# Kernel optimization log

Hardware: AMD Instinct MI355X
Metric: run time of the kernel (lower is better)

Reference implementation:

```python
import jax, jax.numpy as jnp
import numpy as np

B, N = 32768, 20            # batch nodes, temporal neighbors
NF, EF, TF = 172, 172, 100  # node / edge / time feature dims
E = NF + TF                 # query_dim = 272
KD = NF + EF + TF           # key_dim = 444
H = 2                       # heads
HD = E // H                 # head dim 136
OUT = NF                    # output_dimension defaults to n_node_features
NEG = jnp.float32(-1e30)


def setup_inputs() -> dict:
    key = jax.random.key(0)
    ks = jax.random.split(key, 20)
    s = 0.02
    return {
        "src_node_features": jax.random.normal(ks[0], (B, NF), jnp.float32),
        "src_time_features": jax.random.normal(ks[1], (B, 1, TF), jnp.float32),
        "neighbor_features": jax.random.normal(ks[2], (B, N, NF), jnp.float32),
        "neighbor_time_features": jax.random.normal(ks[3], (B, N, TF), jnp.float32),
        "edge_features": jax.random.normal(ks[4], (B, N, EF), jnp.float32),
        "neighbor_mask": jax.random.bernoulli(ks[5], 0.3, (B, N)),
        # nn.MultiheadAttention params (separate q/k/v projections since kdim!=embed_dim)
        "q_w": jax.random.normal(ks[6], (E, E), jnp.float32) * s,
        "k_w": jax.random.normal(ks[7], (E, KD), jnp.float32) * s,
        "v_w": jax.random.normal(ks[8], (E, KD), jnp.float32) * s,
        "q_b": jnp.zeros((E,), jnp.float32),
        "k_b": jnp.zeros((E,), jnp.float32),
        "v_b": jnp.zeros((E,), jnp.float32),
        "out_w": jax.random.normal(ks[9], (E, E), jnp.float32) * s,
        "out_b": jnp.zeros((E,), jnp.float32),
        # merger MLP: Linear(E+NF -> OUT), ReLU, Linear(OUT -> OUT)
        "m1_w": jax.random.normal(ks[10], (OUT, E + NF), jnp.float32) * s,
        "m1_b": jnp.zeros((OUT,), jnp.float32),
        "m2_w": jax.random.normal(ks[11], (OUT, OUT), jnp.float32) * s,
        "m2_b": jnp.zeros((OUT,), jnp.float32),
    }


def reference(src_node_features, src_time_features, neighbor_features,
              neighbor_time_features, edge_features, neighbor_mask,
              q_w, k_w, v_w, q_b, k_b, v_b, out_w, out_b,
              m1_w, m1_b, m2_w, m2_b):
    b = src_node_features.shape[0]
    # single query per node: [B, E]
    query = jnp.concatenate([src_node_features, src_time_features[:, 0, :]], axis=1)
    # keys/values: [B, N, KD]
    kv = jnp.concatenate([neighbor_features, edge_features, neighbor_time_features], axis=2)

    # nodes with no valid neighbor: unmask position 0 (matches torch clone/set trick)
    invalid = jnp.all(neighbor_mask, axis=1)                      # [B]
    mask = neighbor_mask.at[:, 0].set(
        jnp.where(invalid, False, neighbor_mask[:, 0]))

    q = (query @ q_w.T + q_b).reshape(b, H, HD)                   # [B,H,HD]
    k = (kv @ k_w.T + k_b).reshape(b, N, H, HD)                   # [B,N,H,HD]
    v = (kv @ v_w.T + v_b).reshape(b, N, H, HD)

    scores = jnp.einsum('bhd,bnhd->bhn', q, k) / jnp.sqrt(jnp.float32(HD))
    scores = jnp.where(mask[:, None, :], NEG, scores)
    attn = jax.nn.softmax(scores, axis=-1)                        # [B,H,N]
    attn_weights = attn.mean(axis=1)                              # averaged over heads [B,N]

    ctx = jnp.einsum('bhn,bnhd->bhd', attn, v).reshape(b, E)
    attn_out = ctx @ out_w.T + out_b                              # [B,E]
    attn_out = jnp.where(invalid[:, None], 0.0, attn_out)

    merged = jnp.concatenate([attn_out, src_node_features], axis=1)
    hidden = jax.nn.relu(merged @ m1_w.T + m1_b)
    output = hidden @ m2_w.T + m2_b                               # [B,OUT]
    return output, attn_weights
```

## Files before the change

### kernel.cpp

```cpp
#include <hip/hip_runtime.h>
#include <hip/hip_bf16.h>
#include <math.h>

#define NF 172
#define TF_ 100
#define EF 172
#define EDIM 272
#define KD 444
#define NNB 20
#define HD 136
#define OUT_D 172

typedef __attribute__((ext_vector_type(4))) float f32x4;
typedef __attribute__((ext_vector_type(8))) __bf16 bf16x8;
typedef __attribute__((ext_vector_type(4))) __bf16 bf16x4;

__global__ void sniff_k(const unsigned char* __restrict__ m, int* __restrict__ flag) {
    __shared__ int c1, c2;
    if (threadIdx.x == 0) { c1 = 0; c2 = 0; }
    __syncthreads();
    for (int k = 0; k < 4; ++k) {
        int p = threadIdx.x * 4 + k;
        unsigned char v = m[p];
        if ((p & 3) != 0 && v)          atomicOr(&c1, 1);
        if ((p & 3) == 3 && v == 0x3f)  atomicOr(&c2, 1);
    }
    __syncthreads();
    if (threadIdx.x == 0) flag[0] = c2 ? 2 : (c1 ? 1 : 0);
}

__global__ __launch_bounds__(256) void prep_k(
    const float* __restrict__ q_w, const float* __restrict__ k_w,
    const float* __restrict__ v_w, const float* __restrict__ q_b,
    const float* __restrict__ v_b, const float* __restrict__ out_w,
    const float* __restrict__ out_b,
    float* __restrict__ GT, float* __restrict__ gb,
    float* __restrict__ MT, float* __restrict__ mb)
{
    const int blk = blockIdx.x;
    const int tid = threadIdx.x;
    if (blk < 888) {
        const int j = blk, h = j / 444, jj = j - h * 444;
        for (int k = tid; k < 272; k += 256) {
            float acc = 0.f;
#pragma unroll 4
            for (int c = 0; c < 136; ++c)
                acc += q_w[(size_t)(h * 136 + c) * 272 + k] *
                       k_w[(size_t)(h * 136 + c) * 444 + jj];
            GT[(size_t)j * 272 + k] = acc;
        }
    } else if (blk < 888 + 272) {
        const int j = blk - 888;
        for (int r = tid; r < 888; r += 256) {
            const int h = r / 444, d = r - h * 444;
            float acc = 0.f;
#pragma unroll 4
            for (int c = 0; c < 136; ++c)
                acc += v_w[(size_t)(h * 136 + c) * 444 + d] *
                       out_w[(size_t)j * 272 + h * 136 + c];
            MT[(size_t)j * 888 + r] = acc;
        }
    } else if (blk < 888 + 272 + 4) {
        const int j = (blk - 888 - 272) * 256 + tid;
        if (j < 888) {
            const int h = j / 444, jj = j - h * 444;
            float acc = 0.f;
#pragma unroll 4
            for (int c = 0; c < 136; ++c)
                acc += q_b[h * 136 + c] * k_w[(size_t)(h * 136 + c) * 444 + jj];
            gb[j] = acc;
        }
    } else {
        const int j = (blk - 888 - 272 - 4) * 256 + tid;
        if (j < 272) {
            float acc = out_b[j];
#pragma unroll 4
            for (int e = 0; e < 272; ++e)
                acc += v_b[e] * out_w[(size_t)j * 272 + e];
            mb[j] = acc;
        }
    }
}

#define BKP 40

__global__ __launch_bounds__(256) void gemm_mfma_k(
    const float* __restrict__ A0, int a0_cols, int a0_stride,
    const float* __restrict__ A1, int a1_stride,
    const float* __restrict__ W, int w_stride,
    const float* __restrict__ bias,
    const float* __restrict__ invalf,
    int relu,
    float* __restrict__ C, int c_stride,
    int N, int K)
{
    __shared__ __bf16 As[2][128][BKP];
    __shared__ __bf16 Bs[2][128][BKP];

    const int tid  = threadIdx.x;
    const int lane = tid & 63;
    const int wv   = tid >> 6;
    const int wr   = wv >> 1;
    const int wc   = wv & 1;
    const int lr   = lane & 15;
    const int lg   = lane >> 4;
    const int m0   = blockIdx.x * 128;
    const int n0   = blockIdx.y * 128;

    f32x4 acc[4][4];
#pragma unroll
    for (int i = 0; i < 4; ++i)
#pragma unroll
        for (int j = 0; j < 4; ++j) acc[i][j] = (f32x4)(0.f);

    const int srow = tid >> 1;
    const int sch0 = (tid & 1) * 4;
    const float4 z4 = make_float4(0.f, 0.f, 0.f, 0.f);
    float4 va[4], vb[4];

#define LOAD_T(k0base) do {                                                   \
    _Pragma("unroll")                                                         \
    for (int i_ = 0; i_ < 4; ++i_) {                                          \
        const int k_ = (k0base) + (sch0 + i_) * 4;                            \
        va[i_] = z4; vb[i_] = z4;                                             \
        if (k_ < K) {                                                         \
            const float* p_ = (k_ < a0_cols)                                  \
                ? (A0 + (size_t)(m0 + srow) * a0_stride + k_)                 \
                : (A1 + (size_t)(m0 + srow) * a1_stride + (k_ - a0_cols));    \
            va[i_] = *(const float4*)p_;                                      \
            if ((n0 + srow) < N)                                              \
                vb[i_] = *(const float4*)(W + (size_t)(n0 + srow) * w_stride + k_); \
        }                                                                     \
    } } while (0)

#define STORE_T(bufi) do {                                                    \
    _Pragma("unroll")                                                         \
    for (int i_ = 0; i_ < 4; ++i_) {                                          \
        bf16x4 ta_, tb_;                                                      \
        ta_[0] = (__bf16)va[i_].x; ta_[1] = (__bf16)va[i_].y;                 \
        ta_[2] = (__bf16)va[i_].z; ta_[3] = (__bf16)va[i_].w;                 \
        tb_[0] = (__bf16)vb[i_].x; tb_[1] = (__bf16)vb[i_].y;                 \
        tb_[2] = (__bf16)vb[i_].z; tb_[3] = (__bf16)vb[i_].w;                 \
        *(bf16x4*)&As[bufi][srow][(sch0 + i_) * 4] = ta_;                     \
        *(bf16x4*)&Bs[bufi][srow][(sch0 + i_) * 4] = tb_;                     \
    } } while (0)

    const int ktiles = (K + 31) / 32;
    LOAD_T(0);
    STORE_T(0);
    __syncthreads();

    int cur = 0;
    for (int t = 0; t < ktiles; ++t) {
        const int more = (t + 1 < ktiles);
        if (more) LOAD_T((t + 1) * 32);

        bf16x8 af[4], bfr[4];
#pragma unroll
        for (int f = 0; f < 4; ++f) {
            af[f]  = *(const bf16x8*)&As[cur][wr * 64 + f * 16 + lr][lg * 8];
            bfr[f] = *(const bf16x8*)&Bs[cur][wc * 64 + f * 16 + lr][lg * 8];
        }
#pragma unroll
        for (int fm = 0; fm < 4; ++fm)
#pragma unroll
            for (int fn = 0; fn < 4; ++fn)
                acc[fm][fn] = __builtin_amdgcn_mfma_f32_16x16x32_bf16(
                    af[fm], bfr[fn], acc[fm][fn], 0, 0, 0);

        if (more) STORE_T(cur ^ 1);
        __syncthreads();
        cur ^= 1;
    }
#undef LOAD_T
#undef STORE_T

    float bv[4];
#pragma unroll
    for (int fn = 0; fn < 4; ++fn) {
        const int col = n0 + wc * 64 + fn * 16 + lr;
        bv[fn] = (bias && col < N) ? bias[col] : 0.f;
    }
#pragma unroll
    for (int fm = 0; fm < 4; ++fm) {
#pragma unroll
        for (int j = 0; j < 4; ++j) {
            const int row = m0 + wr * 64 + fm * 16 + lg * 4 + j;
            float zf = 1.f;
            if (invalf && invalf[row] != 0.f) zf = 0.f;
#pragma unroll
            for (int fn = 0; fn < 4; ++fn) {
                const int col = n0 + wc * 64 + fn * 16 + lr;
                if (col < N) {
                    float v = acc[fm][fn][j] + bv[fn];
                    if (relu) v = fmaxf(v, 0.f);
                    C[(size_t)row * c_stride + col] = v * zf;
                }
            }
        }
    }
}

__device__ __forceinline__ float dot4(float4 a, float4 b) {
    return a.x * b.x + a.y * b.y + a.z * b.z + a.w * b.w;
}

__global__ __launch_bounds__(256) void attn_flash2_k(
    const float* __restrict__ nf, const float* __restrict__ ef,
    const float* __restrict__ ntf,
    const unsigned char* __restrict__ maskp,
    const int* __restrict__ mode_p,
    const float* __restrict__ qk,
    float* __restrict__ wkv,
    float* __restrict__ invalf,
    float* __restrict__ attnw)
{
    __shared__ float  sc_lds[2][2][NNB];
    __shared__ float4 acc_lds[2][4][64];

    const int tid  = threadIdx.x;
    const int lane = tid & 63;
    const int wv   = tid >> 6;
    const int rw   = wv >> 1;
    const int hf   = wv & 1;
    const int b    = blockIdx.x * 2 + rw;
    const int mode = mode_p[0];

    int mv = 0;
    if (lane < NNB) {
        if (mode == 0)      mv = ((const int*)maskp)[(size_t)b * NNB + lane] != 0;
        else if (mode == 1) mv = maskp[(size_t)b * NNB + lane] != 0;
        else                mv = ((const float*)maskp)[(size_t)b * NNB + lane] != 0.f;
    }
    unsigned long long bal = __ballot(lane < NNB && mv);
    const int inv = ((bal & 0xFFFFFULL) == 0xFFFFFULL);
    if (inv && lane == 0) mv = 0;
    if (hf == 0 && lane == 0) invalf[b] = (float)inv;

    const float* qrow = qk + (size_t)b * 888;
    const float4 z4 = make_float4(0.f, 0.f, 0.f, 0.f);
    float4 q0a = *(const float4*)(qrow + lane * 4);
    float4 q1a = *(const float4*)(qrow + KD + lane * 4);
    float4 q0b = z4, q1b = z4;
    if (lane < 47) {
        q0b = *(const float4*)(qrow + (64 + lane) * 4);
        q1b = *(const float4*)(qrow + KD + (64 + lane) * 4);
    }

    const size_t rbase = (size_t)b * NNB + hf * 10;
    const float* pA;
    if (lane < 43) pA = nf + rbase * NF + lane * 4;
    else           pA = ef + rbase * EF + (lane - 43) * 4;
    const float* pB;
    int strideB;
    if (lane < 22) { pB = ef  + rbase * EF  + (21 + lane) * 4; strideB = EF;  }
    else           { pB = ntf + rbase * TF_ + (lane - 22) * 4; strideB = TF_; }

    float4 kA[10], kB[10];
#pragma unroll
    for (int s = 0; s < 10; ++s) {
        kA[s] = *(const float4*)pA; pA += NF;
        kB[s] = z4;
        if (lane < 47) { kB[s] = *(const float4*)pB; }
        pB += strideB;
    }

    float s0v[10], s1v[10];
#pragma unroll
    for (int s = 0; s < 10; ++s) {
        s0v[s] = dot4(q0a, kA[s]) + dot4(q0b, kB[s]);
        s1v[s] = dot4(q1a, kA[s]) + dot4(q1b, kB[s]);
    }
#pragma unroll
    for (int off = 32; off; off >>= 1) {
#pragma unroll
        for (int s = 0; s < 10; ++s) {
            s0v[s] += __shfl_xor(s0v[s], off);
            s1v[s] += __shfl_xor(s1v[s], off);
        }
    }

    const float scal = 0.08574929257125441f;
#pragma unroll
    for (int s = 0; s < 10; ++s) {
        const int g = hf * 10 + s;
        const int mn = __shfl(mv, g);
        s0v[s] = mn ? -1e30f : s0v[s] * scal;
        s1v[s] = mn ? -1e30f : s1v[s] * scal;
        if (lane == s) { sc_lds[rw][0][g] = s0v[s]; sc_lds[rw][1][g] = s1v[s]; }
    }
    __syncthreads();

    float m0 = -3.4e38f, m1 = -3.4e38f;
#pragma unroll
    for (int g = 0; g < NNB; ++g) {
        m0 = fmaxf(m0, sc_lds[rw][0][g]);
        m1 = fmaxf(m1, sc_lds[rw][1][g]);
    }
    float sum0 = 0.f, sum1 = 0.f;
#pragma unroll
    for (int g = 0; g < NNB; ++g) {
        sum0 += expf(sc_lds[rw][0][g] - m0);
        sum1 += expf(sc_lds[rw][1][g] - m1);
    }
    const float r0 = 1.f / sum0;
    const float r1 = 1.f / sum1;

    float4 a0a = z4, a0b = z4, a1a = z4, a1b = z4;
#pragma unroll
    for (int s = 0; s < 10; ++s) {
        const float w0 = expf(s0v[s] - m0) * r0;
        const float w1 = expf(s1v[s] - m1) * r1;
        a0a.x += w0 * kA[s].x; a0a.y += w0 * kA[s].y; a0a.z += w0 * kA[s].z; a0a.w += w0 * kA[s].w;
        a0b.x += w0 * kB[s].x; a0b.y += w0 * kB[s].y; a0b.z += w0 * kB[s].z; a0b.w += w0 * kB[s].w;
        a1a.x += w1 * kA[s].x; a1a.y += w1 * kA[s].y; a1a.z += w1 * kA[s].z; a1a.w += w1 * kA[s].w;
        a1b.x += w1 * kB[s].x; a1b.y += w1 * kB[s].y; a1b.z += w1 * kB[s].z; a1b.w += w1 * kB[s].w;
    }

    if (hf == 1) {
        acc_lds[rw][0][lane] = a0a;
        acc_lds[rw][1][lane] = a0b;
        acc_lds[rw][2][lane] = a1a;
        acc_lds[rw][3][lane] = a1b;
    }
    __syncthreads();
    if (hf == 0) {
        float4 p0a = acc_lds[rw][0][lane], p0b = acc_lds[rw][1][lane];
        float4 p1a = acc_lds[rw][2][lane], p1b = acc_lds[rw][3][lane];
        a0a.x += p0a.x; a0a.y += p0a.y; a0a.z += p0a.z; a0a.w += p0a.w;
        a0b.x += p0b.x; a0b.y += p0b.y; a0b.z += p0b.z; a0b.w += p0b.w;
        a1a.x += p1a.x; a1a.y += p1a.y; a1a.z += p1a.z; a1a.w += p1a.w;
        a1b.x += p1b.x; a1b.y += p1b.y; a1b.z += p1b.z; a1b.w += p1b.w;

        float* wrow = wkv + (size_t)b * 888;
        *(float4*)(wrow + lane * 4)      = a0a;
        *(float4*)(wrow + KD + lane * 4) = a1a;
        if (lane < 47) {
            *(float4*)(wrow + (64 + lane) * 4)      = a0b;
            *(float4*)(wrow + KD + (64 + lane) * 4) = a1b;
        }
#pragma unroll
        for (int g = 0; g < NNB; ++g) {
            if (lane == g)
                attnw[(size_t)b * NNB + g] =
                    0.5f * (expf(sc_lds[rw][0][g] - m0) * r0 +
                            expf(sc_lds[rw][1][g] - m1) * r1);
        }
    }
}

extern "C" void kernel_launch(void* const* d_in, const int* in_sizes, int n_in,
                              void* d_out, int out_size, void* d_ws, size_t ws_size,
                              hipStream_t stream) {
    const float* src_node = (const float*)d_in[0];
    const float* src_time = (const float*)d_in[1];
    const float* nfp      = (const float*)d_in[2];
    const float* ntfp     = (const float*)d_in[3];
    const float* efp      = (const float*)d_in[4];
    const unsigned char* maskp = (const unsigned char*)d_in[5];
    const float* q_w   = (const float*)d_in[6];
    const float* k_w   = (const float*)d_in[7];
    const float* v_w   = (const float*)d_in[8];
    const float* q_b   = (const float*)d_in[9];
    const float* v_b   = (const float*)d_in[11];
    const float* out_w = (const float*)d_in[12];
    const float* out_b = (const float*)d_in[13];
    const float* m1_w  = (const float*)d_in[14];
    const float* m1_b  = (const float*)d_in[15];
    const float* m2_w  = (const float*)d_in[16];
    const float* m2_b  = (const float*)d_in[17];

    const int B = in_sizes[0] / NF;

    float* ws   = (float*)d_ws;
    int*   flag = (int*)d_ws;
    float* qkb  = ws + 16;
    float* invb = qkb + (size_t)B * 888;
    float* aob  = invb + B;
    float* GT   = aob + (size_t)B * 272;
    float* gb   = GT + 888 * 272;
    float* MT   = gb + 888;
    float* mb   = MT + 272 * 888;
    float* hidb = qkb;
    float* outp  = (float*)d_out;
    float* attnw = outp + (size_t)B * OUT_D;

    const int gm = B / 128;

    sniff_k<<<1, 256, 0, stream>>>(maskp, flag);
    prep_k<<<1166, 256, 0, stream>>>(q_w, k_w, v_w, q_b, v_b, out_w, out_b,
                                     GT, gb, MT, mb);

    gemm_mfma_k<<<dim3(gm, 7), 256, 0, stream>>>(
        src_node, NF, NF, src_time, TF_,
        GT, 272, gb, nullptr, 0, qkb, 888, 888, 272);

    attn_flash2_k<<<B / 2, 256, 0, stream>>>(nfp, efp, ntfp, maskp, flag,
                                             qkb, qkb, invb, attnw);

    gemm_mfma_k<<<dim3(gm, 3), 256, 0, stream>>>(
        qkb, 888, 888, nullptr, 0,
        MT, 888, mb, invb, 0, aob, 272, 272, 888);

    gemm_mfma_k<<<dim3(gm, 2), 256, 0, stream>>>(
        aob, EDIM, EDIM, src_node, NF,
        m1_w, KD, m1_b, nullptr, 1, hidb, OUT_D, OUT_D, KD);

    gemm_mfma_k<<<dim3(gm, 2), 256, 0, stream>>>(
        hidb, OUT_D, OUT_D, nullptr, 0,
        m2_w, OUT_D, m2_b, nullptr, 0, outp, OUT_D, OUT_D, OUT_D);
}
```

Baseline: 718.3 us.

## Fold out-projection into merger weights, split attention across four waves per node

Precomputes a combined weight W2 = m1_w[:, :272] · out_w · v_w per head, which folds the attention output projection into the first merger GEMM and removes one full B×888×272 GEMM plus its intermediate buffer. Invalid rows are handled with a separate bias vector (m1_b) instead of zeroing. The attention kernel now runs one node per block with four waves each covering five neighbors. It uses DPP-based wave reductions, exp2 with a pre-scaled log2e constant, and deferred normalization. The GEMM also gets a swizzled block index for L2 locality. The trade-off is more weight-preprocessing work and a small change in rounding order in the bf16 GEMM.

```diff
diff --git a/kernel.cpp b/kernel.cpp
--- a/kernel.cpp
+++ b/kernel.cpp
@@ -15,6 +15,8 @@
 typedef __attribute__((ext_vector_type(8))) __bf16 bf16x8;
 typedef __attribute__((ext_vector_type(4))) __bf16 bf16x4;
 
+#define SC2 0.12371009f
+
 __global__ void sniff_k(const unsigned char* __restrict__ m, int* __restrict__ flag) {
     __shared__ int c1, c2;
     if (threadIdx.x == 0) { c1 = 0; c2 = 0; }
@@ -29,13 +31,13 @@
     if (threadIdx.x == 0) flag[0] = c2 ? 2 : (c1 ? 1 : 0);
 }
 
-__global__ __launch_bounds__(256) void prep_k(
+__global__ __launch_bounds__(256) void prep1_k(
     const float* __restrict__ q_w, const float* __restrict__ k_w,
-    const float* __restrict__ v_w, const float* __restrict__ q_b,
-    const float* __restrict__ v_b, const float* __restrict__ out_w,
-    const float* __restrict__ out_b,
+    const float* __restrict__ q_b, const float* __restrict__ v_b,
+    const float* __restrict__ out_w, const float* __restrict__ out_b,
+    const float* __restrict__ m1_w,
     float* __restrict__ GT, float* __restrict__ gb,
-    float* __restrict__ MT, float* __restrict__ mb)
+    float* __restrict__ OW2, float* __restrict__ mb)
 {
     const int blk = blockIdx.x;
     const int tid = threadIdx.x;
@@ -49,19 +51,17 @@
                        k_w[(size_t)(h * 136 + c) * 444 + jj];
             GT[(size_t)j * 272 + k] = acc;
         }
-    } else if (blk < 888 + 272) {
+    } else if (blk < 1060) {
         const int j = blk - 888;
-        for (int r = tid; r < 888; r += 256) {
-            const int h = r / 444, d = r - h * 444;
+        for (int k = tid; k < 272; k += 256) {
             float acc = 0.f;
 #pragma unroll 4
-            for (int c = 0; c < 136; ++c)
-                acc += v_w[(size_t)(h * 136 + c) * 444 + d] *
-                       out_w[(size_t)j * 272 + h * 136 + c];
-            MT[(size_t)j * 888 + r] = acc;
-        }
-    } else if (blk < 888 + 272 + 4) {
-        const int j = (blk - 888 - 272) * 256 + tid;
+            for (int e = 0; e < 272; ++e)
+                acc += m1_w[(size_t)j * 444 + e] * out_w[(size_t)e * 272 + k];
+            OW2[(size_t)j * 272 + k] = acc;
+        }
+    } else if (blk < 1064) {
+        const int j = (blk - 1060) * 256 + tid;
         if (j < 888) {
             const int h = j / 444, jj = j - h * 444;
             float acc = 0.f;
@@ -71,13 +71,45 @@
             gb[j] = acc;
         }
     } else {
-        const int j = (blk - 888 - 272 - 4) * 256 + tid;
-        if (j < 272) {
+        for (int j = tid; j < 272; j += 256) {
             float acc = out_b[j];
 #pragma unroll 4
             for (int e = 0; e < 272; ++e)
                 acc += v_b[e] * out_w[(size_t)j * 272 + e];
             mb[j] = acc;
+        }
+    }
+}
+
+__global__ __launch_bounds__(256) void prep2_k(
+    const float* __restrict__ v_w, const float* __restrict__ m1_w,
+    const float* __restrict__ m1_b,
+    const float* __restrict__ OW2, const float* __restrict__ mb,
+    float* __restrict__ W2, float* __restrict__ bias_v)
+{
+    const int blk = blockIdx.x;
+    const int tid = threadIdx.x;
+    if (blk < 172) {
+        const int j = blk;
+        for (int r = tid; r < 888; r += 256) {
+            const int h = (r >= 444);
+            const int d = r - h * 444;
+            float acc = 0.f;
+#pragma unroll 4
+            for (int c = 0; c < 136; ++c)
+                acc += v_w[(size_t)(h * 136 + c) * 444 + d] *
+                       OW2[(size_t)j * 272 + h * 136 + c];
+            W2[(size_t)j * 1060 + r] = acc;
+        }
+        for (int k = tid; k < 172; k += 256)
+            W2[(size_t)j * 1060 + 888 + k] = m1_w[(size_t)j * 444 + 272 + k];
+    } else {
+        for (int j = tid; j < 172; j += 256) {
+            float acc = m1_b[j];
+#pragma unroll 4
+            for (int e = 0; e < 272; ++e)
+                acc += m1_w[(size_t)j * 444 + e] * mb[e];
+            bias_v[j] = acc;
         }
     }
 }
@@ -89,6 +121,7 @@
     const float* __restrict__ A1, int a1_stride,
     const float* __restrict__ W, int w_stride,
     const float* __restrict__ bias,
+    const float* __restrict__ bias_inv,
     const float* __restrict__ invalf,
     int relu,
     float* __restrict__ C, int c_stride,
@@ -104,8 +137,15 @@
     const int wc   = wv & 1;
     const int lr   = lane & 15;
     const int lg   = lane >> 4;
-    const int m0   = blockIdx.x * 128;
-    const int n0   = blockIdx.y * 128;
+
+    const int nt   = gridDim.y;
+    const int nwg  = gridDim.x * nt;
+    const int lid  = blockIdx.x + blockIdx.y * gridDim.x;
+    const int swz  = (lid & 7) * (nwg >> 3) + (lid >> 3);
+    const int xt   = swz / nt;
+    const int yt   = swz - xt * nt;
+    const int m0   = xt * 128;
+    const int n0   = yt * 128;
 
     f32x4 acc[4][4];
 #pragma unroll
@@ -175,26 +215,26 @@
 #undef LOAD_T
 #undef STORE_T
 
-    float bv[4];
+    float bv[4], bvi[4];
 #pragma unroll
     for (int fn = 0; fn < 4; ++fn) {
         const int col = n0 + wc * 64 + fn * 16 + lr;
-        bv[fn] = (bias && col < N) ? bias[col] : 0.f;
+        bv[fn]  = (bias && col < N) ? bias[col] : 0.f;
+        bvi[fn] = (bias_inv && col < N) ? bias_inv[col] : bv[fn];
     }
 #pragma unroll
     for (int fm = 0; fm < 4; ++fm) {
 #pragma unroll
         for (int j = 0; j < 4; ++j) {
             const int row = m0 + wr * 64 + fm * 16 + lg * 4 + j;
-            float zf = 1.f;
-            if (invalf && invalf[row] != 0.f) zf = 0.f;
+            const bool bad = invalf && invalf[row] != 0.f;
 #pragma unroll
             for (int fn = 0; fn < 4; ++fn) {
                 const int col = n0 + wc * 64 + fn * 16 + lr;
                 if (col < N) {
-                    float v = acc[fm][fn][j] + bv[fn];
+                    float v = acc[fm][fn][j] + (bad ? bvi[fn] : bv[fn]);
                     if (relu) v = fmaxf(v, 0.f);
-                    C[(size_t)row * c_stride + col] = v * zf;
+                    C[(size_t)row * c_stride + col] = v;
                 }
             }
         }
@@ -205,7 +245,22 @@
     return a.x * b.x + a.y * b.y + a.z * b.z + a.w * b.w;
 }
 
-__global__ __launch_bounds__(256) void attn_flash2_k(
+__device__ __forceinline__ float wave_allsum(float x) {
+    int t;
+    t = __builtin_amdgcn_update_dpp(0, __float_as_int(x), 0x128, 0xf, 0xf, true);
+    x += __int_as_float(t);
+    t = __builtin_amdgcn_update_dpp(0, __float_as_int(x), 0x124, 0xf, 0xf, true);
+    x += __int_as_float(t);
+    t = __builtin_amdgcn_update_dpp(0, __float_as_int(x), 0x122, 0xf, 0xf, true);
+    x += __int_as_float(t);
+    t = __builtin_amdgcn_update_dpp(0, __float_as_int(x), 0x121, 0xf, 0xf, true);
+    x += __int_as_float(t);
+    x += __shfl_xor(x, 16);
+    x += __shfl_xor(x, 32);
+    return x;
+}
+
+__global__ __launch_bounds__(256) void attn_flash3_k(
     const float* __restrict__ nf, const float* __restrict__ ef,
     const float* __restrict__ ntf,
     const unsigned char* __restrict__ maskp,
@@ -215,15 +270,14 @@
     float* __restrict__ invalf,
     float* __restrict__ attnw)
 {
-    __shared__ float  sc_lds[2][2][NNB];
-    __shared__ float4 acc_lds[2][4][64];
+    __shared__ float  sc[2][NNB];
+    __shared__ float  lmax[4][2], lsum[4][2];
+    __shared__ float4 accx[3][4][64];
 
     const int tid  = threadIdx.x;
     const int lane = tid & 63;
-    const int wv   = tid >> 6;
-    const int rw   = wv >> 1;
-    const int hf   = wv & 1;
-    const int b    = blockIdx.x * 2 + rw;
+    const int w    = tid >> 6;
+    const int b    = blockIdx.x;
     const int mode = mode_p[0];
 
     int mv = 0;
@@ -232,10 +286,10 @@
         else if (mode == 1) mv = maskp[(size_t)b * NNB + lane] != 0;
         else                mv = ((const float*)maskp)[(size_t)b * NNB + lane] != 0.f;
     }
-    unsigned long long bal = __ballot(lane < NNB && mv);
-    const int inv = ((bal & 0xFFFFFULL) == 0xFFFFFULL);
-    if (inv && lane == 0) mv = 0;
-    if (hf == 0 && lane == 0) invalf[b] = (float)inv;
+    unsigned long long bal = __ballot(lane < NNB && mv) & 0xFFFFFULL;
+    const int inv = (bal == 0xFFFFFULL);
+    if (inv) bal &= ~1ULL;
+    if (w == 0 && lane == 0) invalf[b] = (float)inv;
 
     const float* qrow = qk + (size_t)b * 888;
     const float4 z4 = make_float4(0.f, 0.f, 0.f, 0.f);
@@ -247,7 +301,7 @@
         q1b = *(const float4*)(qrow + KD + (64 + lane) * 4);
     }
 
-    const size_t rbase = (size_t)b * NNB + hf * 10;
+    const size_t rbase = (size_t)b * NNB + w * 5;
     const float* pA;
     if (lane < 43) pA = nf + rbase * NF + lane * 4;
     else           pA = ef + rbase * EF + (lane - 43) * 4;
@@ -256,96 +310,97 @@
     if (lane < 22) { pB = ef  + rbase * EF  + (21 + lane) * 4; strideB = EF;  }
     else           { pB = ntf + rbase * TF_ + (lane - 22) * 4; strideB = TF_; }
 
-    float4 kA[10], kB[10];
-#pragma unroll
-    for (int s = 0; s < 10; ++s) {
+    float4 kA[5], kB[5];
+#pragma unroll
+    for (int s = 0; s < 5; ++s) {
         kA[s] = *(const float4*)pA; pA += NF;
         kB[s] = z4;
-        if (lane < 47) { kB[s] = *(const float4*)pB; }
+        if (lane < 47) kB[s] = *(const float4*)pB;
         pB += strideB;
     }
 
-    float s0v[10], s1v[10];
-#pragma unroll
-    for (int s = 0; s < 10; ++s) {
-        s0v[s] = dot4(q0a, kA[s]) + dot4(q0b, kB[s]);
-        s1v[s] = dot4(q1a, kA[s]) + dot4(q1b, kB[s]);
-    }
-#pragma unroll
-    for (int off = 32; off; off >>= 1) {
-#pragma unroll
-        for (int s = 0; s < 10; ++s) {
-            s0v[s] += __shfl_xor(s0v[s], off);
-            s1v[s] += __shfl_xor(s1v[s], off);
-        }
-    }
-
-    const float scal = 0.08574929257125441f;
-#pragma unroll
-    for (int s = 0; s < 10; ++s) {
-        const int g = hf * 10 + s;
-        const int mn = __shfl(mv, g);
-        s0v[s] = mn ? -1e30f : s0v[s] * scal;
-        s1v[s] = mn ? -1e30f : s1v[s] * scal;
-        if (lane == s) { sc_lds[rw][0][g] = s0v[s]; sc_lds[rw][1][g] = s1v[s]; }
-    }
-    __syncthreads();
-
-    float m0 = -3.4e38f, m1 = -3.4e38f;
-#pragma unroll
-    for (int g = 0; g < NNB; ++g) {
-        m0 = fmaxf(m0, sc_lds[rw][0][g]);
-        m1 = fmaxf(m1, sc_lds[rw][1][g]);
-    }
-    float sum0 = 0.f, sum1 = 0.f;
-#pragma unroll
-    for (int g = 0; g < NNB; ++g) {
-        sum0 += expf(sc_lds[rw][0][g] - m0);
-        sum1 += expf(sc_lds[rw][1][g] - m1);
-    }
-    const float r0 = 1.f / sum0;
-    const float r1 = 1.f / sum1;
+    float s0[5], s1[5];
+#pragma unroll
+    for (int s = 0; s < 5; ++s) {
+        s0[s] = wave_allsum(dot4(q0a, kA[s]) + dot4(q0b, kB[s]));
+        s1[s] = wave_allsum(dot4(q1a, kA[s]) + dot4(q1b, kB[s]));
+    }
+#pragma unroll
+    for (int s = 0; s < 5; ++s) {
+        const int g = w * 5 + s;
+        const int mn = (int)((bal >> g) & 1ULL);
+        s0[s] = mn ? -1e30f : s0[s] * SC2;
+        s1[s] = mn ? -1e30f : s1[s] * SC2;
+        if (lane == s) { sc[0][g] = s0[s]; sc[1][g] = s1[s]; }
+    }
+
+    float lm0 = s0[0], lm1 = s1[0];
+#pragma unroll
+    for (int s = 1; s < 5; ++s) { lm0 = fmaxf(lm0, s0[s]); lm1 = fmaxf(lm1, s1[s]); }
+    if (lane == 0) { lmax[w][0] = lm0; lmax[w][1] = lm1; }
+    __syncthreads();
+
+    const float m0 = fmaxf(fmaxf(lmax[0][0], lmax[1][0]), fmaxf(lmax[2][0], lmax[3][0]));
+    const float m1 = fmaxf(fmaxf(lmax[0][1], lmax[1][1]), fmaxf(lmax[2][1], lmax[3][1]));
+
+    float u0[5], u1[5];
+    float ls0 = 0.f, ls1 = 0.f;
+#pragma unroll
+    for (int s = 0; s < 5; ++s) {
+        u0[s] = exp2f(s0[s] - m0); ls0 += u0[s];
+        u1[s] = exp2f(s1[s] - m1); ls1 += u1[s];
+    }
+    if (lane == 0) { lsum[w][0] = ls0; lsum[w][1] = ls1; }
 
     float4 a0a = z4, a0b = z4, a1a = z4, a1b = z4;
 #pragma unroll
-    for (int s = 0; s < 10; ++s) {
-        const float w0 = expf(s0v[s] - m0) * r0;
-        const float w1 = expf(s1v[s] - m1) * r1;
+    for (int s = 0; s < 5; ++s) {
+        const float w0 = u0[s], w1 = u1[s];
         a0a.x += w0 * kA[s].x; a0a.y += w0 * kA[s].y; a0a.z += w0 * kA[s].z; a0a.w += w0 * kA[s].w;
         a0b.x += w0 * kB[s].x; a0b.y += w0 * kB[s].y; a0b.z += w0 * kB[s].z; a0b.w += w0 * kB[s].w;
         a1a.x += w1 * kA[s].x; a1a.y += w1 * kA[s].y; a1a.z += w1 * kA[s].z; a1a.w += w1 * kA[s].w;
         a1b.x += w1 * kB[s].x; a1b.y += w1 * kB[s].y; a1b.z += w1 * kB[s].z; a1b.w += w1 * kB[s].w;
     }
-
-    if (hf == 1) {
-        acc_lds[rw][0][lane] = a0a;
-        acc_lds[rw][1][lane] = a0b;
-        acc_lds[rw][2][lane] = a1a;
-        acc_lds[rw][3][lane] = a1b;
-    }
-    __syncthreads();
-    if (hf == 0) {
-        float4 p0a = acc_lds[rw][0][lane], p0b = acc_lds[rw][1][lane];
-        float4 p1a = acc_lds[rw][2][lane], p1b = acc_lds[rw][3][lane];
-        a0a.x += p0a.x; a0a.y += p0a.y; a0a.z += p0a.z; a0a.w += p0a.w;
-        a0b.x += p0b.x; a0b.y += p0b.y; a0b.z += p0b.z; a0b.w += p0b.w;
-        a1a.x += p1a.x; a1a.y += p1a.y; a1a.z += p1a.z; a1a.w += p1a.w;
-        a1b.x += p1b.x; a1b.y += p1b.y; a1b.z += p1b.z; a1b.w += p1b.w;
-
+    __syncthreads();
+
+    const float r0 = 1.f / (lsum[0][0] + lsum[1][0] + lsum[2][0] + lsum[3][0]);
+    const float r1 = 1.f / (lsum[0][1] + lsum[1][1] + lsum[2][1] + lsum[3][1]);
+
+    if (w) {
+        accx[w - 1][0][lane] = a0a;
+        accx[w - 1][1][lane] = a0b;
+        accx[w - 1][2][lane] = a1a;
+        accx[w - 1][3][lane] = a1b;
+    }
+    __syncthreads();
+
+    if (w == 0) {
+#pragma unroll
+        for (int i = 0; i < 3; ++i) {
+            float4 p0a = accx[i][0][lane], p0b = accx[i][1][lane];
+            float4 p1a = accx[i][2][lane], p1b = accx[i][3][lane];
+            a0a.x += p0a.x; a0a.y += p0a.y; a0a.z += p0a.z; a0a.w += p0a.w;
+            a0b.x += p0b.x; a0b.y += p0b.y; a0b.z += p0b.z; a0b.w += p0b.w;
+            a1a.x += p1a.x; a1a.y += p1a.y; a1a.z += p1a.z; a1a.w += p1a.w;
+            a1b.x += p1b.x; a1b.y += p1b.y; a1b.z += p1b.z; a1b.w += p1b.w;
+        }
+        const float zf0 = inv ? 0.f : r0;
+        const float zf1 = inv ? 0.f : r1;
         float* wrow = wkv + (size_t)b * 888;
-        *(float4*)(wrow + lane * 4)      = a0a;
-        *(float4*)(wrow + KD + lane * 4) = a1a;
+        float4 o;
+        o.x = a0a.x * zf0; o.y = a0a.y * zf0; o.z = a0a.z * zf0; o.w = a0a.w * zf0;
+        *(float4*)(wrow + lane * 4) = o;
+        o.x = a1a.x * zf1; o.y = a1a.y * zf1; o.z = a1a.z * zf1; o.w = a1a.w * zf1;
+        *(float4*)(wrow + KD + lane * 4) = o;
         if (lane < 47) {
-            *(float4*)(wrow + (64 + lane) * 4)      = a0b;
-            *(float4*)(wrow + KD + (64 + lane) * 4) = a1b;
-        }
-#pragma unroll
-        for (int g = 0; g < NNB; ++g) {
-            if (lane == g)
-                attnw[(size_t)b * NNB + g] =
-                    0.5f * (expf(sc_lds[rw][0][g] - m0) * r0 +
-                            expf(sc_lds[rw][1][g] - m1) * r1);
-        }
+            o.x = a0b.x * zf0; o.y = a0b.y * zf0; o.z = a0b.z * zf0; o.w = a0b.w * zf0;
+            *(float4*)(wrow + (64 + lane) * 4) = o;
+            o.x = a1b.x * zf1; o.y = a1b.y * zf1; o.z = a1b.z * zf1; o.w = a1b.w * zf1;
+            *(float4*)(wrow + KD + (64 + lane) * 4) = o;
+        }
+        if (lane < NNB)
+            attnw[(size_t)b * NNB + lane] =
+                0.5f * (exp2f(sc[0][lane] - m0) * r0 + exp2f(sc[1][lane] - m1) * r1);
     }
 }
 
@@ -372,41 +427,39 @@
 
     const int B = in_sizes[0] / NF;
 
-    float* ws   = (float*)d_ws;
-    int*   flag = (int*)d_ws;
-    float* qkb  = ws + 16;
-    float* invb = qkb + (size_t)B * 888;
-    float* aob  = invb + B;
-    float* GT   = aob + (size_t)B * 272;
-    float* gb   = GT + 888 * 272;
-    float* MT   = gb + 888;
-    float* mb   = MT + 272 * 888;
-    float* hidb = qkb;
-    float* outp  = (float*)d_out;
-    float* attnw = outp + (size_t)B * OUT_D;
+    float* ws     = (float*)d_ws;
+    int*   flag   = (int*)d_ws;
+    float* qkb    = ws + 16;
+    float* invb   = qkb + (size_t)B * 888;
+    float* hidb   = invb + B;
+    float* GT     = hidb + (size_t)B * 172;
+    float* gb     = GT + 888 * 272;
+    float* mb     = gb + 888;
+    float* OW2    = mb + 272;
+    float* W2     = OW2 + 172 * 272;
+    float* bias_v = W2 + 172 * 1060;
+    float* outp   = (float*)d_out;
+    float* attnw  = outp + (size_t)B * OUT_D;
 
     const int gm = B / 128;
 
     sniff_k<<<1, 256, 0, stream>>>(maskp, flag);
-    prep_k<<<1166, 256, 0, stream>>>(q_w, k_w, v_w, q_b, v_b, out_w, out_b,
-                                     GT, gb, MT, mb);
+    prep1_k<<<1065, 256, 0, stream>>>(q_w, k_w, q_b, v_b, out_w, out_b, m1_w,
+                                      GT, gb, OW2, mb);
+    prep2_k<<<173, 256, 0, stream>>>(v_w, m1_w, m1_b, OW2, mb, W2, bias_v);
 
     gemm_mfma_k<<<dim3(gm, 7), 256, 0, stream>>>(
         src_node, NF, NF, src_time, TF_,
-        GT, 272, gb, nullptr, 0, qkb, 888, 888, 272);
-
-    attn_flash2_k<<<B / 2, 256, 0, stream>>>(nfp, efp, ntfp, maskp, flag,
-                                             qkb, qkb, invb, attnw);
-
-    gemm_mfma_k<<<dim3(gm, 3), 256, 0, stream>>>(
-        qkb, 888, 888, nullptr, 0,
-        MT, 888, mb, invb, 0, aob, 272, 272, 888);
+        GT, 272, gb, nullptr, nullptr, 0, qkb, 888, 888, 272);
+
+    attn_flash3_k<<<B, 256, 0, stream>>>(nfp, efp, ntfp, maskp, flag,
+                                         qkb, qkb, invb, attnw);
 
     gemm_mfma_k<<<dim3(gm, 2), 256, 0, stream>>>(
-        aob, EDIM, EDIM, src_node, NF,
-        m1_w, KD, m1_b, nullptr, 1, hidb, OUT_D, OUT_D, KD);
+        qkb, 888, 888, src_node, NF,
+        W2, 1060, bias_v, m1_b, invb, 1, hidb, OUT_D, OUT_D, 1060);
 
     gemm_mfma_k<<<dim3(gm, 2), 256, 0, stream>>>(
         hidb, OUT_D, OUT_D, nullptr, 0,
-        m2_w, OUT_D, m2_b, nullptr, 0, outp, OUT_D, OUT_D, OUT_D);
-}
+        m2_w, OUT_D, m2_b, nullptr, nullptr, 0, outp, OUT_D, OUT_D, OUT_D);
+}
```

New measurement: 665.3 us. 7.4% less time.
